# Kernel optimization log

Hardware: AMD Instinct MI355X
Metric: run time of the kernel (lower is better)

Reference implementation:

```python
import jax, jax.numpy as jnp
import numpy as np

NEIGHBOR = 9
PAD = (NEIGHBOR - 1) // 2  # 4


def setup_inputs() -> dict:
    key = jax.random.key(0)
    k1, k2 = jax.random.split(key)
    B, C, H, W = 32, 3, 512, 512
    x = jax.random.normal(k1, (B, C, H, W), dtype=jnp.float32)
    p = jax.random.uniform(k2, (B, 1, H, W), dtype=jnp.float32)
    return {"x": x, "p": p}


def reference(x, p):
    # filter = ones(3, 3, 9, 9) / 9**2  (OIHW) — sums box mean over ALL 3 input
    # channels into each output channel, exactly as torch F.conv2d does here.
    filt = jnp.ones((3, 3, NEIGHBOR, NEIGHBOR), dtype=x.dtype) / (NEIGHBOR ** 2)
    mean_normal = jax.lax.conv_general_dilated(
        x, filt,
        window_strides=(1, 1),
        padding=[(PAD, PAD), (PAD, PAD)],
        dimension_numbers=("NCHW", "OIHW", "NCHW"),
    )
    return p * x + (1.0 - p) * mean_normal
```

## Files before the change

### kernel.cpp

```cpp
#include <hip/hip_runtime.h>


#define TX 64
#define TY 64
#define HALO 4
#define THW (TY + 2 * HALO)
#define TWW (TX + 2 * HALO)

__global__ __launch_bounds__(256) void reflection_fusion_kernel(
    const float* __restrict__ x, const float* __restrict__ p,
    float* __restrict__ out, int B, int H, int W) {
  __shared__ float csum[THW][TWW];
  __shared__ float hsum[THW][TX];

  const int tid = threadIdx.x;
  const int b = blockIdx.z;
  const int x0 = blockIdx.x * TX;
  const int y0 = blockIdx.y * TY;
  const long HW = (long)H * W;
  const float* xb = x + (long)b * 3 * HW;

  for (int i = tid; i < THW * TWW; i += 256) {
    int r = i / TWW;
    int cc = i - r * TWW;
    int gy = y0 + r - HALO;
    int gx = x0 + cc - HALO;
    float s = 0.f;
    if (gy >= 0 && gy < H && gx >= 0 && gx < W) {
      long base = (long)gy * W + gx;
      s = xb[base] + xb[base + HW] + xb[base + 2 * HW];
    }
    csum[r][cc] = s;
  }
  __syncthreads();

  for (int i = tid; i < THW * TX; i += 256) {
    int r = i >> 6;
    int cc = i & (TX - 1);
    float s = 0.f;
#pragma unroll
    for (int k = 0; k < 9; ++k) s += csum[r][cc + k];
    hsum[r][cc] = s;
  }
  __syncthreads();

  const float inv81 = 1.0f / 81.0f;
  const int cc = tid & 63;
  const int r0 = tid >> 6;
#pragma unroll
  for (int it = 0; it < 16; ++it) {
    int rr = r0 + it * 4;
    float s = 0.f;
#pragma unroll
    for (int k = 0; k < 9; ++k) s += hsum[rr + k][cc];
    float m = s * inv81;
    int gy = y0 + rr;
    int gx = x0 + cc;
    long pix = (long)gy * W + gx;
    float pv = p[(long)b * HW + pix];
    float om = 1.0f - pv;
#pragma unroll
    for (int c = 0; c < 3; ++c) {
      float xv = xb[(long)c * HW + pix];
      out[((long)b * 3 + c) * HW + pix] = pv * xv + om * m;
    }
  }
}

extern "C" void kernel_launch(void* const* d_in, const int* in_sizes, int n_in,
                              void* d_out, int out_size, void* d_ws, size_t ws_size,
                              hipStream_t stream) {
  const float* x = (const float*)d_in[0];
  const float* p = (const float*)d_in[1];
  float* out = (float*)d_out;

  const int H = 512, W = 512;
  const int B = in_sizes[1] / (H * W);

  dim3 grid(W / TX, H / TY, B);
  dim3 block(256);
  reflection_fusion_kernel<<<grid, block, 0, stream>>>(x, p, out, B, H, W);
}
```

Before: 216.1 us.

## Vectorize halo loads and compute vertical box sum with per-thread sliding window

The tile load now reads float4 chunks of the three channels instead of scalars. The hsum shared buffer and one barrier are removed. Each thread computes horizontal sums for 24 rows into registers and slides a running vertical sum over 16 contiguous rows. This trades redundant horizontal-sum work (24 rows per 16 outputs) and higher register use for fewer shared memory round trips and less synchronization. The float4 boundary check zeroes a whole chunk if it is partly out of range, which is only correct because the width is a multiple of 4.

```diff
diff --git a/kernel.cpp b/kernel.cpp
--- a/kernel.cpp
+++ b/kernel.cpp
@@ -9,9 +9,8 @@
 
 __global__ __launch_bounds__(256) void reflection_fusion_kernel(
     const float* __restrict__ x, const float* __restrict__ p,
-    float* __restrict__ out, int B, int H, int W) {
-  __shared__ float csum[THW][TWW];
-  __shared__ float hsum[THW][TX];
+    float* __restrict__ out, int H, int W) {
+  __shared__ __align__(16) float csum[THW][TWW];
 
   const int tid = threadIdx.x;
   const int b = blockIdx.z;
@@ -19,51 +18,67 @@
   const int y0 = blockIdx.y * TY;
   const long HW = (long)H * W;
   const float* xb = x + (long)b * 3 * HW;
+  const float* pb = p + (long)b * HW;
+  float* ob = out + (long)b * 3 * HW;
 
-  for (int i = tid; i < THW * TWW; i += 256) {
-    int r = i / TWW;
-    int cc = i - r * TWW;
-    int gy = y0 + r - HALO;
-    int gx = x0 + cc - HALO;
-    float s = 0.f;
-    if (gy >= 0 && gy < H && gx >= 0 && gx < W) {
-      long base = (long)gy * W + gx;
-      s = xb[base] + xb[base + HW] + xb[base + 2 * HW];
+  const int NCHUNK = THW * (TWW / 4);
+#pragma unroll
+  for (int pass = 0; pass < 6; ++pass) {
+    int i = tid + pass * 256;
+    if (i < NCHUNK) {
+      int r = (unsigned)i / 18u;
+      int j = i - r * 18;
+      int gy = y0 + r - HALO;
+      int gx = x0 + 4 * j - HALO;
+      float4 s = make_float4(0.f, 0.f, 0.f, 0.f);
+      if ((unsigned)gy < (unsigned)H && gx >= 0 && gx + 4 <= W) {
+        const float* base = xb + (long)gy * W + gx;
+        float4 a = *(const float4*)(base);
+        float4 c1 = *(const float4*)(base + HW);
+        float4 c2 = *(const float4*)(base + 2 * HW);
+        s.x = a.x + c1.x + c2.x;
+        s.y = a.y + c1.y + c2.y;
+        s.z = a.z + c1.z + c2.z;
+        s.w = a.w + c1.w + c2.w;
+      }
+      *(float4*)&csum[r][4 * j] = s;
     }
-    csum[r][cc] = s;
   }
   __syncthreads();
 
-  for (int i = tid; i < THW * TX; i += 256) {
-    int r = i >> 6;
-    int cc = i & (TX - 1);
-    float s = 0.f;
+  const int cc = tid & 63;
+  const int rg = tid >> 6;
+  const int rbase = rg * 16;
+
+  float h[24];
 #pragma unroll
-    for (int k = 0; k < 9; ++k) s += csum[r][cc + k];
-    hsum[r][cc] = s;
+  for (int k = 0; k < 24; ++k) {
+    const float* row = &csum[rbase + k][cc];
+    float s = row[0];
+#pragma unroll
+    for (int d = 1; d < 9; ++d) s += row[d];
+    h[k] = s;
   }
-  __syncthreads();
 
   const float inv81 = 1.0f / 81.0f;
-  const int cc = tid & 63;
-  const int r0 = tid >> 6;
+  float s = 0.f;
+#pragma unroll
+  for (int k = 0; k < 9; ++k) s += h[k];
+
 #pragma unroll
   for (int it = 0; it < 16; ++it) {
-    int rr = r0 + it * 4;
-    float s = 0.f;
-#pragma unroll
-    for (int k = 0; k < 9; ++k) s += hsum[rr + k][cc];
+    if (it > 0) s += h[it + 8] - h[it - 1];
+    int gy = y0 + rbase + it;
+    long pix = (long)gy * W + (x0 + cc);
+    float pv = pb[pix];
     float m = s * inv81;
-    int gy = y0 + rr;
-    int gx = x0 + cc;
-    long pix = (long)gy * W + gx;
-    float pv = p[(long)b * HW + pix];
     float om = 1.0f - pv;
-#pragma unroll
-    for (int c = 0; c < 3; ++c) {
-      float xv = xb[(long)c * HW + pix];
-      out[((long)b * 3 + c) * HW + pix] = pv * xv + om * m;
-    }
+    float v0 = xb[pix];
+    float v1 = xb[HW + pix];
+    float v2 = xb[2 * HW + pix];
+    ob[pix] = pv * v0 + om * m;
+    ob[HW + pix] = pv * v1 + om * m;
+    ob[2 * HW + pix] = pv * v2 + om * m;
   }
 }
 
@@ -79,5 +94,5 @@
 
   dim3 grid(W / TX, H / TY, B);
   dim3 block(256);
-  reflection_fusion_kernel<<<grid, block, 0, stream>>>(x, p, out, B, H, W);
+  reflection_fusion_kernel<<<grid, block, 0, stream>>>(x, p, out, H, W);
 }
```

After: 215.6 us. Within noise of the previous version (-0.2%).
